# Optimization experiments

Measured on AMD Instinct MI355X. Metric: run time of the kernel, lower is better.

## Reference

```python
import jax, jax.numpy as jnp
import numpy as np

NC = 10          # tess_size (number of tessellation cells on [0,1])
D = NC - 1       # CPA parameter dim with zero boundary
EPS = 1e-7
N = 2097152      # number of 2D points
MASK = jnp.array([1, 0])  # left=True coupling mask

def _make_basis(nc):
    # Continuous piecewise-affine velocity on [0,1]: cell c has v(x)=a_c*x+b_c.
    # Constraints: continuity at interior knots + zero boundary v(0)=v(1)=0.
    L = np.zeros((nc + 1, 2 * nc))
    for k in range(1, nc):
        xk = k / nc
        L[k - 1, 2 * (k - 1)] = xk; L[k - 1, 2 * (k - 1) + 1] = 1.0
        L[k - 1, 2 * k] = -xk;      L[k - 1, 2 * k + 1] = -1.0
    L[nc - 1, 1] = 1.0                                        # v(0) = 0
    L[nc, 2 * (nc - 1)] = 1.0; L[nc, 2 * (nc - 1) + 1] = 1.0  # v(1) = 0
    _, _, Vt = np.linalg.svd(L)
    return jnp.asarray(Vt[nc + 1:].T, dtype=jnp.float32)      # (2*nc, D) null-space basis (svd)

_B = _make_basis(NC)

def cpab_flow(x, theta):
    """Integrate dphi/dt = v(phi), t in [0,1], v CPA parameterized by theta.
    x: (N,1) in [0,1], theta: (N,D). Returns (phi(x,1), dphi/dx), each (N,1).
    Closed-form per-cell integration with cell hopping (<= NC hops, fixed scan).
    dphi/dx = exp(sum_c a_c * dt_c) (analytic space gradient)."""
    A = (theta @ _B.T).reshape(-1, NC, 2)          # (N, NC, 2): (a_c, b_c)
    xp = x[:, 0]
    c0 = jnp.clip((xp * NC).astype(jnp.int32), 0, NC - 1)
    carry0 = (xp, jnp.ones_like(xp), c0, jnp.zeros_like(xp))

    def step(carry, _):
        phi, t, c, ld = carry
        a = jnp.take_along_axis(A[:, :, 0], c[:, None], 1)[:, 0]
        b = jnp.take_along_axis(A[:, :, 1], c[:, None], 1)[:, 0]
        v = a * phi + b
        lin = jnp.abs(a) < 1e-10
        sa = jnp.where(lin, 1.0, a)
        xc = jnp.where(v >= 0, (c + 1).astype(phi.dtype), c.astype(phi.dtype)) / NC
        den = phi + b / sa
        den = jnp.where(jnp.abs(den) < 1e-30, 1e-30, den)
        t_exp = jnp.log(jnp.maximum((xc + b / sa) / den, 1e-30)) / sa
        sb = jnp.where(jnp.abs(b) < 1e-30, 1.0, b)
        thit = jnp.where(lin, (xc - phi) / sb, t_exp)
        thit = jnp.where(jnp.abs(v) < 1e-14, jnp.inf, thit)   # fixed point: never leaves cell
        cross = thit < t
        dt = jnp.where(cross, thit, t)
        phi_new = jnp.where(lin, phi + b * dt,
                            (phi + b / sa) * jnp.exp(a * dt) - b / sa)
        phi_new = jnp.where(cross, xc, phi_new)               # snap to knot when hopping
        active = t > 0
        phi = jnp.where(active, phi_new, phi)
        ld = ld + jnp.where(active, a * dt, 0.0)              # accumulate log dphi/dx
        t = jnp.where(active, t - dt, t)
        c = jnp.where(active & cross,
                      jnp.clip(c + jnp.where(v >= 0, 1, -1), 0, NC - 1), c)
        return (phi, t, c, ld), None

    (phi, _, _, ld), _ = jax.lax.scan(step, carry0, None, length=NC)
    return phi[:, None], jnp.exp(ld)[:, None]

def mlp(h, p):
    # Linear -> (Linear, ReLU) x 2 -> Linear  (matches torch MLP(hidden_layers=3))
    h = h @ p[0] + p[1]
    h = jax.nn.relu(h @ p[2] + p[3])
    h = jax.nn.relu(h @ p[4] + p[5])
    return h @ p[6] + p[7]

def setup_inputs():
    key = jax.random.key(0)
    ks = jax.random.split(key, 17)
    inp = {"x": jax.random.uniform(ks[0], (N, 2), dtype=jnp.float32)}
    shapes = [(1, 10), (10,), (10, 10), (10,), (10, 10), (10,), (10, D), (D,)]
    names = ["w0", "b0", "w1", "b1", "w2", "b2", "w3", "b3"]
    i = 1
    for pref in ("m1", "m2"):
        for nm, sh in zip(names, shapes):
            scale = 0.3 if len(sh) == 2 else 0.1
            inp[pref + nm] = jax.random.normal(ks[i], sh, dtype=jnp.float32) * scale
            i += 1
    return inp

def reference(x, m1w0, m1b0, m1w1, m1b1, m1w2, m1b2, m1w3, m1b3,
              m2w0, m2b0, m2w1, m2b1, m2w2, m2b2, m2w3, m2b3):
    x = jnp.clip(x, EPS, 1.0 - EPS)
    xs = x[:, MASK]                        # index_select with coupling mask
    x1, x2 = xs[:, 0:1], xs[:, 1:2]
    theta2 = mlp(x1, (m2w0, m2b0, m2w1, m2b1, m2w2, m2b2, m2w3, m2b3))
    z2, g2 = cpab_flow(x2, theta2)
    theta1 = mlp(z2, (m1w0, m1b0, m1w1, m1b1, m1w2, m1b2, m1w3, m1b3))
    z1, g1 = cpab_flow(x1, theta1)
    z = jnp.concatenate([z1, z2], axis=1)[:, MASK]
    log_dz_dx = jnp.log(jnp.concatenate([g1, g2], axis=1))[:, MASK]
    return z, log_dz_dx
```

## Files before the change

kernel.cpp:

```cpp
#include <hip/hip_runtime.h>
#include <cmath>

#define THREADS 256
#define NCELL 10
#define DDIM 9

typedef float f32x2 __attribute__((ext_vector_type(2)));

__device__ __forceinline__ f32x2 fma2(f32x2 a, f32x2 b, f32x2 c) {
  return __builtin_elementwise_fma(a, b, c);
}
__device__ __forceinline__ f32x2 max2(f32x2 a, f32x2 b) {
  return __builtin_elementwise_max(a, b);
}

struct Basis { float Bt[DDIM][2 * NCELL]; };

static void compute_basis_host(Basis* bs) {
  double L[11][20];
  for (int r = 0; r < 11; ++r)
    for (int c = 0; c < 20; ++c) L[r][c] = 0.0;
  for (int k = 1; k < NCELL; ++k) {
    double xk = (double)k / (double)NCELL;
    L[k - 1][2 * (k - 1)] = xk;
    L[k - 1][2 * (k - 1) + 1] = 1.0;
    L[k - 1][2 * k] = -xk;
    L[k - 1][2 * k + 1] = -1.0;
  }
  L[NCELL - 1][1] = 1.0;
  L[NCELL][2 * (NCELL - 1)] = 1.0;
  L[NCELL][2 * (NCELL - 1) + 1] = 1.0;

  double v[11][20];
  double tau[11];
  for (int i = 0; i < 11; ++i) {
    double alpha = L[i][i];
    double xn2 = 0.0;
    for (int l = i + 1; l < 20; ++l) xn2 += L[i][l] * L[i][l];
    double xnorm = sqrt(xn2);
    for (int l = 0; l < 20; ++l) v[i][l] = 0.0;
    v[i][i] = 1.0;
    if (xnorm == 0.0) {
      tau[i] = 0.0;
    } else {
      double beta = sqrt(alpha * alpha + xn2);
      if (alpha >= 0.0) beta = -beta;
      tau[i] = (beta - alpha) / beta;
      double sc = 1.0 / (alpha - beta);
      for (int l = i + 1; l < 20; ++l) v[i][l] = L[i][l] * sc;
      L[i][i] = beta;
      for (int j = i + 1; j < 11; ++j) {
        double w = 0.0;
        for (int l = i; l < 20; ++l) w += L[j][l] * v[i][l];
        w *= tau[i];
        for (int l = i; l < 20; ++l) L[j][l] -= w * v[i][l];
      }
    }
  }
  for (int j = 11; j < 20; ++j) {
    double q[20];
    for (int l = 0; l < 20; ++l) q[l] = 0.0;
    q[j] = 1.0;
    for (int i = 10; i >= 0; --i) {
      double w = 0.0;
      for (int l = i; l < 20; ++l) w += v[i][l] * q[l];
      w *= tau[i];
      for (int l = i; l < 20; ++l) q[l] -= w * v[i][l];
    }
    for (int l = 0; l < 20; ++l) bs->Bt[j - 11][l] = (float)q[l];
  }
}

__global__ void fold_kernel(
    const float* __restrict__ w0_1, const float* __restrict__ b0_1,
    const float* __restrict__ w1_1, const float* __restrict__ b1_1,
    const float* __restrict__ w3_1, const float* __restrict__ b3_1,
    const float* __restrict__ w0_2, const float* __restrict__ b0_2,
    const float* __restrict__ w1_2, const float* __restrict__ b1_2,
    const float* __restrict__ w3_2, const float* __restrict__ b3_2,
    float* __restrict__ ws, Basis bb) {
  for (int f = threadIdx.x; f < 260; f += THREADS) {
    int m = f / 130;
    int j = f % 130;
    const float* w0 = (m == 0) ? w0_1 : w0_2;
    const float* b0 = (m == 0) ? b0_1 : b0_2;
    const float* w1 = (m == 0) ? w1_1 : w1_2;
    const float* w3 = (m == 0) ? w3_1 : w3_2;
    const float* b3 = (m == 0) ? b3_1 : b3_2;
    const float* b1 = (m == 0) ? b1_1 : b1_2;
    float val = 0.0f;
    if (j < 10) {
      for (int r = 0; r < 10; ++r) val += w0[r] * w1[r * 10 + j];
    } else if (j < 20) {
      int jj = j - 10;
      for (int r = 0; r < 10; ++r) val += b0[r] * w1[r * 10 + jj];
      val += b1[jj];
    } else if (j < 120) {
      int jj = j - 20;
      int r = jj / 10, k = jj % 10;
      if (k < 9) {
        float g = (float)(k + 1) * 0.1f;
        for (int t = 0; t < DDIM; ++t)
          val += w3[r * DDIM + t] * (bb.Bt[t][2 * (k + 1)] * g + bb.Bt[t][2 * (k + 1) + 1]);
      }
    } else {
      int k = j - 120;
      if (k < 9) {
        float g = (float)(k + 1) * 0.1f;
        for (int t = 0; t < DDIM; ++t)
          val += b3[t] * (bb.Bt[t][2 * (k + 1)] * g + bb.Bt[t][2 * (k + 1) + 1]);
      }
    }
    ws[f] = val;
  }
}

__device__ __forceinline__ void mlp_A(float xin,
    const float* __restrict__ w2, const float* __restrict__ b2,
    const float* __restrict__ wbf,
    f32x2* abcol, float& amin) {
  const f32x2* W01 = (const f32x2*)wbf;
  const f32x2* B01 = W01 + 5;
  const f32x2* W3V = W01 + 10;
  const f32x2* B3V = W01 + 60;
  const f32x2* w2p = (const f32x2*)w2;
  const f32x2* b2p = (const f32x2*)b2;

  f32x2 h1[5], h2[5];
  f32x2 xx = {xin, xin};
  f32x2 zero = {0.0f, 0.0f};
#pragma unroll
  for (int p = 0; p < 5; ++p) h1[p] = max2(fma2(xx, W01[p], B01[p]), zero);

#pragma unroll
  for (int p = 0; p < 5; ++p) h2[p] = b2p[p];
#pragma unroll
  for (int r = 0; r < 10; ++r) {
    float h = h1[r >> 1][r & 1];
    f32x2 hh = {h, h};
#pragma unroll
    for (int p = 0; p < 5; ++p) h2[p] = fma2(hh, w2p[r * 5 + p], h2[p]);
  }
#pragma unroll
  for (int p = 0; p < 5; ++p) h2[p] = max2(h2[p], zero);

  f32x2 vp[5];
#pragma unroll
  for (int p = 0; p < 5; ++p) vp[p] = B3V[p];
#pragma unroll
  for (int r = 0; r < 10; ++r) {
    float h = h2[r >> 1][r & 1];
    f32x2 hh = {h, h};
#pragma unroll
    for (int p = 0; p < 5; ++p) vp[p] = fma2(hh, W3V[r * 5 + p], vp[p]);
  }

  float v[NCELL + 1];
  v[0] = 0.0f;
#pragma unroll
  for (int k = 1; k <= NCELL; ++k) v[k] = vp[(k - 1) >> 1][(k - 1) & 1];

  float mn = 1e30f;
#pragma unroll
  for (int c = 0; c < NCELL; ++c) {
    float ac = (v[c + 1] - v[c]) * 10.0f;
    float bc = fmaf(ac, -(float)c * 0.1f, v[c]);
    f32x2 ab; ab[0] = ac; ab[1] = bc;
    abcol[c * THREADS] = ab;
    mn = fminf(mn, fabsf(ac));
  }
  amin = mn;
}

__device__ __forceinline__ void flow_dev(float x0, const f32x2* abcol,
                                         bool has_lin, float& zo, float& ldo) {
  int c = (int)(x0 * 10.0f);
  c = c < 0 ? 0 : (c > 9 ? 9 : c);
  f32x2 ab = abcol[c * THREADS];
  float a = ab[0], b = ab[1];
  float v0 = fmaf(a, x0, b);
  bool right = (v0 >= 0.0f);
  float d01 = right ? 0.1f : -0.1f;
  int dirI = right ? 1 : -1;
  float xc = (float)(right ? (c + 1) : c) * 0.1f;
  float rv0 = __builtin_amdgcn_rcpf(v0);
  float rv = rv0;
  bool tiny = fabsf(v0) < 1e-14f;
  float ra = __builtin_amdgcn_rcpf(a);
  float phiC = x0;
  float t = 1.0f;
  bool cross = false;

  int cn = c + dirI; cn = cn < 0 ? 0 : (cn > 9 ? 9 : cn);
  f32x2 abn = abcol[cn * THREADS];
  float ran = __builtin_amdgcn_rcpf(abn[0]);

  for (int it = 0; it < NCELL; ++it) {
    float vxc = fmaf(a, xc, b);
    float ratio = fmaxf(vxc * rv, 1e-30f);
    float l = __logf(ratio);
    float thit = l * ra;
    if (has_lin) {
      bool lin = fabsf(a) < 1e-10f;
      float sb = (fabsf(b) < 1e-30f) ? 1.0f : b;
      float tl = (xc - phiC) * __builtin_amdgcn_rcpf(sb);
      thit = lin ? tl : thit;
    }
    cross = (thit < t) && !tiny;
    t = cross ? (t - thit) : t;
    phiC = cross ? xc : phiC;
    float rvn = __builtin_amdgcn_rcpf(vxc);
    rv = cross ? rvn : rv;
    tiny = cross ? (fabsf(vxc) < 1e-14f) : tiny;
    a = cross ? abn[0] : a;
    b = cross ? abn[1] : b;
    ra = cross ? ran : ra;
    xc = cross ? (xc + d01) : xc;
    c = cross ? cn : c;
    if (__all(!cross)) break;
    int cnn = c + dirI; cnn = cnn < 0 ? 0 : (cnn > 9 ? 9 : cnn);
    abn = abcol[cnn * THREADS];
    ran = __builtin_amdgcn_rcpf(abn[0]);
    cn = cnn;
  }
  bool done = !cross;
  float vterm = fmaf(a, phiC, b);
  float ld = __logf(fmaxf(vterm * rv0, 1e-30f));
  bool linf = fabsf(a) < 1e-10f;
  float rsaf = __builtin_amdgcn_rcpf(linf ? 1.0f : a);
  float bsa = b * rsaf;
  float E = __expf(a * t);
  float pnl = fmaf(phiC + bsa, E, -bsa);
  float pli = fmaf(b, t, phiC);
  float p1 = linf ? pli : pnl;
  zo = done ? p1 : phiC;
  ldo = ld + (done ? a * t : 0.0f);
}

__global__ __launch_bounds__(THREADS, 4) void cpab2d_kernel(
    const float* __restrict__ x,
    const float* __restrict__ m1w2, const float* __restrict__ m1b2,
    const float* __restrict__ m2w2, const float* __restrict__ m2b2,
    const float* __restrict__ wsf,
    float* __restrict__ out, int n) {
  __shared__ f32x2 AB[NCELL][THREADS];
  int i = blockIdx.x * THREADS + threadIdx.x;
  if (i >= n) return;

  float2 xi = reinterpret_cast<const float2*>(x)[i];
  float x2v = fminf(fmaxf(xi.x, 1e-7f), 1.0f - 1e-7f);
  float x1v = fminf(fmaxf(xi.y, 1e-7f), 1.0f - 1e-7f);

  f32x2* abcol = &AB[0][threadIdx.x];
  float amin;

  mlp_A(x1v, m2w2, m2b2, wsf + 130, abcol, amin);
  bool hl2 = __any(amin < 1e-10f);
  float z2, ld2;
  flow_dev(x2v, abcol, hl2, z2, ld2);

  mlp_A(z2, m1w2, m1b2, wsf, abcol, amin);
  bool hl1 = __any(amin < 1e-10f);
  float z1, ld1;
  flow_dev(x1v, abcol, hl1, z1, ld1);

  reinterpret_cast<float2*>(out)[i] = make_float2(z2, z1);
  reinterpret_cast<float2*>(out + 2 * (size_t)n)[i] = make_float2(ld2, ld1);
}

extern "C" void kernel_launch(void* const* d_in, const int* in_sizes, int n_in,
                              void* d_out, int out_size, void* d_ws, size_t ws_size,
                              hipStream_t stream) {
  const float* x    = (const float*)d_in[0];
  const float* m1w0 = (const float*)d_in[1];
  const float* m1b0 = (const float*)d_in[2];
  const float* m1w1 = (const float*)d_in[3];
  const float* m1b1 = (const float*)d_in[4];
  const float* m1w2 = (const float*)d_in[5];
  const float* m1b2 = (const float*)d_in[6];
  const float* m1w3 = (const float*)d_in[7];
  const float* m1b3 = (const float*)d_in[8];
  const float* m2w0 = (const float*)d_in[9];
  const float* m2b0 = (const float*)d_in[10];
  const float* m2w1 = (const float*)d_in[11];
  const float* m2b1 = (const float*)d_in[12];
  const float* m2w2 = (const float*)d_in[13];
  const float* m2b2 = (const float*)d_in[14];
  const float* m2w3 = (const float*)d_in[15];
  const float* m2b3 = (const float*)d_in[16];
  float* out = (float*)d_out;
  float* wsf = (float*)d_ws;
  int n = in_sizes[0] / 2;

  Basis bs;
  compute_basis_host(&bs);

  fold_kernel<<<1, THREADS, 0, stream>>>(
      m1w0, m1b0, m1w1, m1b1, m1w3, m1b3,
      m2w0, m2b0, m2w1, m2b1, m2w3, m2b3, wsf, bs);

  dim3 grid((n + THREADS - 1) / THREADS), block(THREADS);
  cpab2d_kernel<<<grid, block, 0, stream>>>(
      x, m1w2, m1b2, m2w2, m2b2, wsf, out, n);
}
```

Baseline: 45.82 us.

## Reformulate CPA flow in knot-velocity/log2 form with fast path and slow fallback

```diff
diff --git a/kernel.cpp b/kernel.cpp
--- a/kernel.cpp
+++ b/kernel.cpp
@@ -4,6 +4,10 @@
 #define THREADS 256
 #define NCELL 10
 #define DDIM 9
+
+#define LN2F 0.69314718056f
+#define K10L 14.426950408889634f
+#define LIN_THR_L 1.442695e-10f
 
 typedef float f32x2 __attribute__((ext_vector_type(2)));
 
@@ -118,7 +122,7 @@
 __device__ __forceinline__ void mlp_A(float xin,
     const float* __restrict__ w2, const float* __restrict__ b2,
     const float* __restrict__ wbf,
-    f32x2* abcol, float& amin) {
+    f32x2* abcol, float& aminL, float& bmin) {
   const f32x2* W01 = (const f32x2*)wbf;
   const f32x2* B01 = W01 + 5;
   const f32x2* W3V = W01 + 10;
@@ -160,68 +164,150 @@
 #pragma unroll
   for (int k = 1; k <= NCELL; ++k) v[k] = vp[(k - 1) >> 1][(k - 1) & 1];
 
-  float mn = 1e30f;
+  float amn = 1e30f, bmn = 1e30f;
 #pragma unroll
   for (int c = 0; c < NCELL; ++c) {
-    float ac = (v[c + 1] - v[c]) * 10.0f;
-    float bc = fmaf(ac, -(float)c * 0.1f, v[c]);
-    f32x2 ab; ab[0] = ac; ab[1] = bc;
+    float aL = (v[c + 1] - v[c]) * K10L;
+    f32x2 ab; ab[0] = aL; ab[1] = v[c];
     abcol[c * THREADS] = ab;
-    mn = fminf(mn, fabsf(ac));
-  }
-  amin = mn;
-}
-
-__device__ __forceinline__ void flow_dev(float x0, const f32x2* abcol,
-                                         bool has_lin, float& zo, float& ldo) {
-  int c = (int)(x0 * 10.0f);
-  c = c < 0 ? 0 : (c > 9 ? 9 : c);
-  f32x2 ab = abcol[c * THREADS];
-  float a = ab[0], b = ab[1];
-  float v0 = fmaf(a, x0, b);
+    amn = fminf(amn, fabsf(aL));
+    if (c >= 1) bmn = fminf(bmn, fabsf(v[c]));
+  }
+  aminL = amn;
+  bmin = bmn;
+}
+
+__device__ __forceinline__ void flow_fast(float x0, const f32x2* abcol,
+                                          int c0, float aL0, float v0,
+                                          float& zo, float& ldo) {
+  bool right = (v0 >= 0.0f);
+  float d01L = right ? 0.1f * LN2F : -0.1f * LN2F;
+  int dirI = right ? 1 : -1;
+  float c0f = (float)c0;
+  float xc0 = (right ? c0f + 1.0f : c0f) * 0.1f;
+
+  float rv0 = __builtin_amdgcn_rcpf(v0);
+  float rv = rv0;
+  float aL = aL0;
+  float raL = __builtin_amdgcn_rcpf(aL);
+  float ventry = v0;
+  float t = 1.0f;
+  int c = c0;
+  bool cross;
+
+  int cn = c + dirI; cn = cn < 0 ? 0 : (cn > 9 ? 9 : cn);
+  float aLn = abcol[cn * THREADS][0];
+  float ran = __builtin_amdgcn_rcpf(aLn);
+
+  {
+    float dxL = (xc0 - x0) * LN2F;
+    float vxc = fmaf(aL, dxL, ventry);
+    float ratio = fmaxf(vxc * rv, 1e-30f);
+    float thit = __log2f(ratio) * raL;
+    cross = thit < t;
+    t = cross ? t - thit : t;
+    ventry = cross ? vxc : ventry;
+    float rvn = __builtin_amdgcn_rcpf(vxc);
+    rv = cross ? rvn : rv;
+    aL = cross ? aLn : aL;
+    raL = cross ? ran : raL;
+    c = cross ? cn : c;
+  }
+  if (!__all(!cross)) {
+    cn = c + dirI; cn = cn < 0 ? 0 : (cn > 9 ? 9 : cn);
+    aLn = abcol[cn * THREADS][0];
+    ran = __builtin_amdgcn_rcpf(aLn);
+    for (int it = 1; it < NCELL; ++it) {
+      float vxc = fmaf(aL, d01L, ventry);
+      float ratio = fmaxf(vxc * rv, 1e-30f);
+      float thit = __log2f(ratio) * raL;
+      cross = cross && (thit < t);
+      t = cross ? t - thit : t;
+      ventry = cross ? vxc : ventry;
+      float rvn = __builtin_amdgcn_rcpf(vxc);
+      rv = cross ? rvn : rv;
+      aL = cross ? aLn : aL;
+      raL = cross ? ran : raL;
+      c = cross ? cn : c;
+      if (__all(!cross)) break;
+      cn = c + dirI; cn = cn < 0 ? 0 : (cn > 9 ? 9 : cn);
+      aLn = abcol[cn * THREADS][0];
+      ran = __builtin_amdgcn_rcpf(aLn);
+    }
+  }
+  float aF = aL * LN2F;
+  bool moved = t != 1.0f;
+  float ceF = (float)(right ? c : c + 1) * 0.1f;
+  float x_e = moved ? ceF : x0;
+  float bF = fmaf(-aF, x_e, ventry);
+  float rsa = __builtin_amdgcn_rcpf(aF);
+  float bsa = bF * rsa;
+  float E = __expf(aF * t);
+  float z = fmaf(x_e + bsa, E, -bsa);
+  bool done = !cross;
+  z = done ? z : x_e;
+  float ld = __logf(fmaxf(ventry * rv0, 1e-30f));
+  ld += done ? aF * t : 0.0f;
+  zo = z;
+  ldo = ld;
+}
+
+__device__ __noinline__ void flow_slow(float x0, const f32x2* abcol,
+                                       int c0, float aL0, float v0,
+                                       float& zo, float& ldo) {
   bool right = (v0 >= 0.0f);
   float d01 = right ? 0.1f : -0.1f;
   int dirI = right ? 1 : -1;
-  float xc = (float)(right ? (c + 1) : c) * 0.1f;
+  float a = aL0 * LN2F;
+  float b = fmaf(-a, (float)c0 * 0.1f, abcol[c0 * THREADS][1]);
+  float xc = (float)(right ? (c0 + 1) : c0) * 0.1f;
   float rv0 = __builtin_amdgcn_rcpf(v0);
   float rv = rv0;
   bool tiny = fabsf(v0) < 1e-14f;
-  float ra = __builtin_amdgcn_rcpf(a);
+  bool lin = fabsf(a) < 1e-10f;
+  float ra = __builtin_amdgcn_rcpf(lin ? 1.0f : a);
   float phiC = x0;
   float t = 1.0f;
   bool cross = false;
+  int c = c0;
 
   int cn = c + dirI; cn = cn < 0 ? 0 : (cn > 9 ? 9 : cn);
-  f32x2 abn = abcol[cn * THREADS];
-  float ran = __builtin_amdgcn_rcpf(abn[0]);
+  f32x2 sn = abcol[cn * THREADS];
+  float an = sn[0] * LN2F;
+  float bn = fmaf(-an, (float)cn * 0.1f, sn[1]);
+  bool linn = fabsf(an) < 1e-10f;
+  float ran = __builtin_amdgcn_rcpf(linn ? 1.0f : an);
 
   for (int it = 0; it < NCELL; ++it) {
     float vxc = fmaf(a, xc, b);
     float ratio = fmaxf(vxc * rv, 1e-30f);
     float l = __logf(ratio);
     float thit = l * ra;
-    if (has_lin) {
-      bool lin = fabsf(a) < 1e-10f;
+    if (lin) {
       float sb = (fabsf(b) < 1e-30f) ? 1.0f : b;
-      float tl = (xc - phiC) * __builtin_amdgcn_rcpf(sb);
-      thit = lin ? tl : thit;
+      thit = (xc - phiC) * __builtin_amdgcn_rcpf(sb);
     }
-    cross = (thit < t) && !tiny;
+    thit = tiny ? __builtin_inff() : thit;
+    bool crN = (thit < t);
+    cross = (it == 0) ? crN : (cross && crN);
     t = cross ? (t - thit) : t;
     phiC = cross ? xc : phiC;
     float rvn = __builtin_amdgcn_rcpf(vxc);
     rv = cross ? rvn : rv;
     tiny = cross ? (fabsf(vxc) < 1e-14f) : tiny;
-    a = cross ? abn[0] : a;
-    b = cross ? abn[1] : b;
+    a = cross ? an : a;
+    b = cross ? bn : b;
+    lin = cross ? linn : lin;
     ra = cross ? ran : ra;
     xc = cross ? (xc + d01) : xc;
     c = cross ? cn : c;
     if (__all(!cross)) break;
-    int cnn = c + dirI; cnn = cnn < 0 ? 0 : (cnn > 9 ? 9 : cnn);
-    abn = abcol[cnn * THREADS];
-    ran = __builtin_amdgcn_rcpf(abn[0]);
-    cn = cnn;
+    cn = c + dirI; cn = cn < 0 ? 0 : (cn > 9 ? 9 : cn);
+    sn = abcol[cn * THREADS];
+    an = sn[0] * LN2F;
+    bn = fmaf(-an, (float)cn * 0.1f, sn[1]);
+    linn = fabsf(an) < 1e-10f;
+    ran = __builtin_amdgcn_rcpf(linn ? 1.0f : an);
   }
   bool done = !cross;
   float vterm = fmaf(a, phiC, b);
@@ -237,6 +323,23 @@
   ldo = ld + (done ? a * t : 0.0f);
 }
 
+__device__ __forceinline__ void flow_dev(float x0, const f32x2* abcol,
+                                         float aminL, float bmin,
+                                         float& zo, float& ldo) {
+  int c0 = (int)(x0 * 10.0f);
+  c0 = c0 < 0 ? 0 : (c0 > 9 ? 9 : c0);
+  f32x2 s0 = abcol[c0 * THREADS];
+  float aL0 = s0[0], vL0 = s0[1];
+  float dxL = (x0 - (float)c0 * 0.1f) * LN2F;
+  float v0 = fmaf(aL0, dxL, vL0);
+  bool risky = (aminL < LIN_THR_L) || (bmin < 1e-12f) || (fabsf(v0) < 1e-12f);
+  if (__any(risky)) {
+    flow_slow(x0, abcol, c0, aL0, v0, zo, ldo);
+  } else {
+    flow_fast(x0, abcol, c0, aL0, v0, zo, ldo);
+  }
+}
+
 __global__ __launch_bounds__(THREADS, 4) void cpab2d_kernel(
     const float* __restrict__ x,
     const float* __restrict__ m1w2, const float* __restrict__ m1b2,
@@ -252,17 +355,15 @@
   float x1v = fminf(fmaxf(xi.y, 1e-7f), 1.0f - 1e-7f);
 
   f32x2* abcol = &AB[0][threadIdx.x];
-  float amin;
-
-  mlp_A(x1v, m2w2, m2b2, wsf + 130, abcol, amin);
-  bool hl2 = __any(amin < 1e-10f);
+  float aminL, bmin;
+
+  mlp_A(x1v, m2w2, m2b2, wsf + 130, abcol, aminL, bmin);
   float z2, ld2;
-  flow_dev(x2v, abcol, hl2, z2, ld2);
-
-  mlp_A(z2, m1w2, m1b2, wsf, abcol, amin);
-  bool hl1 = __any(amin < 1e-10f);
+  flow_dev(x2v, abcol, aminL, bmin, z2, ld2);
+
+  mlp_A(z2, m1w2, m1b2, wsf, abcol, aminL, bmin);
   float z1, ld1;
-  flow_dev(x1v, abcol, hl1, z1, ld1);
+  flow_dev(x1v, abcol, aminL, bmin, z1, ld1);
 
   reinterpret_cast<float2*>(out)[i] = make_float2(z2, z1);
   reinterpret_cast<float2*>(out + 2 * (size_t)n)[i] = make_float2(ld2, ld1);
```

New measurement: 42.91 us. 6.3% less time.
